# Kernel tuning notes

Measured on AMD Instinct MI355X. Metric: run time of the kernel, lower is better.

Reference implementation:

```python
import jax, jax.numpy as jnp
import numpy as np

FEAT_DIM = 128
GUIDE_DIM = 128
HIDDEN = [1024, 512, 256, 128]
OUT_DIM = 2


def make_coord(shape):
    # grid-center coords in (-1, 1), matching the torch make_coord
    seqs = [(-1.0 + 1.0 / n) + (2.0 / n) * jnp.arange(n, dtype=jnp.float32) for n in shape]
    yy, xx = jnp.meshgrid(seqs[0], seqs[1], indexing='ij')
    return jnp.stack([yy, xx], axis=-1)  # [h, w, 2]


def grid_sample_nearest(img, coord):
    # img: [B, C, H, W]; coord: [B, N, 2] with coord[...,0] along H, coord[...,1] along W
    # replicates F.grid_sample(img, coord.flip(-1)..., mode='nearest', align_corners=False,
    # padding_mode='zeros') followed by permute -> [B, N, C]
    B, C, H, W = img.shape
    iy = jnp.round(((coord[..., 0] + 1.0) * H - 1.0) * 0.5)
    ix = jnp.round(((coord[..., 1] + 1.0) * W - 1.0) * 0.5)
    valid = (iy >= 0) & (iy < H) & (ix >= 0) & (ix < W)
    iyc = jnp.clip(iy, 0, H - 1).astype(jnp.int32)
    ixc = jnp.clip(ix, 0, W - 1).astype(jnp.int32)
    g = jax.vmap(lambda im, y, x: im[:, y, x])(img, iyc, ixc)  # [B, C, N]
    g = g * valid[:, None, :].astype(img.dtype)  # zero padding outside
    return jnp.transpose(g, (0, 2, 1))  # [B, N, C]


def mlp(x, params):
    for W, b in params[:-1]:
        x = jax.nn.relu(x @ W + b)
    W, b = params[-1]
    return x @ W + b


def setup_inputs() -> dict:
    key = jax.random.key(0)
    ks = jax.random.split(key, 16)
    B, h, w = 4, 64, 64
    H_hr = W_hr = 256
    N = H_hr * W_hr  # 65536 query points
    feat = jax.random.normal(ks[0], (B, FEAT_DIM, h, w), jnp.float32)
    coord = jax.random.uniform(ks[1], (B, N, 2), jnp.float32, minval=-1.0, maxval=1.0)
    hr_guide = jax.random.normal(ks[2], (B, GUIDE_DIM, H_hr, W_hr), jnp.float32)
    lr_guide = jax.random.normal(ks[3], (B, GUIDE_DIM, h, w), jnp.float32)
    in_dim = FEAT_DIM + 2 * GUIDE_DIM + 2  # 386
    dims = [in_dim] + HIDDEN + [OUT_DIM]
    inp = {"feat": feat, "coord": coord, "hr_guide": hr_guide, "lr_guide": lr_guide}
    for i in range(len(dims) - 1):
        scale = 1.0 / np.sqrt(dims[i]).astype(np.float32)
        inp[f"W{i}"] = jax.random.normal(ks[4 + 2 * i], (dims[i], dims[i + 1]), jnp.float32) * scale
        inp[f"b{i}"] = jnp.zeros((dims[i + 1],), jnp.float32)
    return inp


def reference(feat, coord, hr_guide, lr_guide, W0, b0, W1, b1, W2, b2, W3, b3, W4, b4):
    params = [(W0, b0), (W1, b1), (W2, b2), (W3, b3), (W4, b4)]
    B, C, h, w = feat.shape
    N = coord.shape[1]
    fc = make_coord((h, w))  # [h, w, 2]
    feat_coord = jnp.broadcast_to(jnp.transpose(fc, (2, 0, 1))[None], (B, 2, h, w))
    q_guide_hr = grid_sample_nearest(hr_guide, coord)  # [B, N, G]
    rx = 1.0 / h
    ry = 1.0 / w
    hw = jnp.array([h, w], dtype=coord.dtype)
    preds = []
    for vx in (-1.0, 1.0):
        for vy in (-1.0, 1.0):
            shift = jnp.array([vx * rx, vy * ry], dtype=coord.dtype)
            coord_ = coord + shift
            q_feat = grid_sample_nearest(feat, coord_)        # [B, N, C]
            q_coord = grid_sample_nearest(feat_coord, coord_)  # [B, N, 2]
            rel_coord = (coord - q_coord) * hw                 # [B, N, 2]
            q_guide_lr = grid_sample_nearest(lr_guide, coord_)  # [B, N, G]
            inp = jnp.concatenate([q_feat, q_guide_hr, q_guide_hr - q_guide_lr, rel_coord], axis=-1)
            pred = mlp(inp.reshape(B * N, -1), params).reshape(B, N, OUT_DIM)
            preds.append(pred)
    preds = jnp.stack(preds, axis=-1)  # [B, N, 2, 4]
    weight = jax.nn.softmax(preds[:, :, 1, :], axis=-1)  # [B, N, 4]
    ret = jnp.sum(preds[:, :, 0, :] * weight, axis=-1, keepdims=True)  # [B, N, 1]
    return ret
```

## Files before the change

### kernel.cpp

```cpp
#include <hip/hip_runtime.h>
#include <cstdint>
#include <cstddef>


typedef unsigned short u16;
typedef unsigned int u32;
typedef _Float16 half8 __attribute__((ext_vector_type(8)));
typedef float floatx4 __attribute__((ext_vector_type(4)));
typedef float floatx2 __attribute__((ext_vector_type(2)));
typedef u32 u32x2 __attribute__((ext_vector_type(2)));
typedef u32 u32x4 __attribute__((ext_vector_type(4)));

__device__ __forceinline__ u16 f2h(float x) {
    _Float16 h = (_Float16)x;
    return __builtin_bit_cast(unsigned short, h);
}
__device__ __forceinline__ float h2f(u16 u) {
    return (float)__builtin_bit_cast(_Float16, u);
}

__device__ __forceinline__ void cp_async16(const void* gsrc, void* lds) {
#if defined(__has_builtin) && __has_builtin(__builtin_amdgcn_global_load_lds)
    __builtin_amdgcn_global_load_lds(
        (__attribute__((address_space(1))) void*)(uintptr_t)gsrc,
        (__attribute__((address_space(3))) void*)(uint32_t)(uintptr_t)lds,
        16, 0, 0);
#else
    *(u32x4*)lds = *(const u32x4*)gsrc;
#endif
}

__global__ void transpose_chw_hwc(const float* __restrict__ src,
                                  u16* __restrict__ dst, int HW) {
    __shared__ float t[32][33];
    const int b = blockIdx.z;
    const int hw0 = blockIdx.x * 32, c0 = blockIdx.y * 32;
    const float* s = src + (size_t)b * 128 * HW;
    u16* d = dst + (size_t)b * HW * 128;
    const int tx = threadIdx.x, ty = threadIdx.y;
#pragma unroll
    for (int j = 0; j < 4; ++j)
        t[ty + j * 8][tx] = s[(size_t)(c0 + ty + j * 8) * HW + hw0 + tx];
    __syncthreads();
#pragma unroll
    for (int j = 0; j < 4; ++j)
        d[(size_t)(hw0 + ty + j * 8) * 128 + c0 + tx] = f2h(t[tx][ty + j * 8]);
}

__global__ void prep_wt(const float* __restrict__ W, u16* __restrict__ Wt,
                        int K, int N, int perm) {
    int idx = blockIdx.x * 256 + threadIdx.x;
    if (idx >= N * K) return;
    int nn = idx / K, kk = idx - nn * K;
    int ka = kk;
    if (perm) {
        int s = kk & 63;
        ka = (kk & ~63) + ((s & 3) << 4) + (s >> 2);
    }
    Wt[idx] = f2h(W[(size_t)ka * N + nn]);
}

__global__ __launch_bounds__(256) void gather_build(
    const float* __restrict__ coord, const u16* __restrict__ hrT,
    const u16* __restrict__ featT, const u16* __restrict__ lrT,
    u16* __restrict__ X, float* __restrict__ rel, int p0) {
    const int wid = threadIdx.x >> 6, lane = threadIdx.x & 63;
    const int pl = blockIdx.x * 4 + wid;
    const int p = p0 + pl;
    const int b = p >> 16;
    const float cy = coord[(size_t)p * 2];
    const float cx = coord[(size_t)p * 2 + 1];
    const u32* hr32 = (const u32*)hrT;
    const u32* ft32 = (const u32*)featT;
    const u32* lr32 = (const u32*)lrT;

    float fy = rintf(((cy + 1.0f) * 256.0f - 1.0f) * 0.5f);
    float fx = rintf(((cx + 1.0f) * 256.0f - 1.0f) * 0.5f);
    bool vh = (fy >= 0.0f) && (fy < 256.0f) && (fx >= 0.0f) && (fx < 256.0f);
    int iy = (int)fminf(fmaxf(fy, 0.0f), 255.0f);
    int ix = (int)fminf(fmaxf(fx, 0.0f), 255.0f);
    u32 hrv = hr32[((((size_t)b * 256 + iy) * 256 + ix) * 128 >> 1) + lane];
    if (!vh) hrv = 0u;
    const float hr_lo = h2f((u16)(hrv & 0xffffu));
    const float hr_hi = h2f((u16)(hrv >> 16));

    const size_t rowbase = (size_t)pl * 4;
#pragma unroll
    for (int s = 0; s < 4; ++s) {
        float sy = (s & 2) ? 0.015625f : -0.015625f;
        float sx = (s & 1) ? 0.015625f : -0.015625f;
        float gy = rintf(((cy + sy + 1.0f) * 64.0f - 1.0f) * 0.5f);
        float gx = rintf(((cx + sx + 1.0f) * 64.0f - 1.0f) * 0.5f);
        bool v = (gy >= 0.0f) && (gy < 64.0f) && (gx >= 0.0f) && (gx < 64.0f);
        int jy = (int)fminf(fmaxf(gy, 0.0f), 63.0f);
        int jx = (int)fminf(fmaxf(gx, 0.0f), 63.0f);
        size_t g32 = ((((size_t)b * 64 + jy) * 64 + jx) * 128 >> 1) + lane;
        u32 fv = ft32[g32];
        u32 lv = lr32[g32];
        if (!v) { fv = 0u; lv = 0u; }
        u16 d_lo = f2h(hr_lo - h2f((u16)(lv & 0xffffu)));
        u16 d_hi = f2h(hr_hi - h2f((u16)(lv >> 16)));

        u32* xr = (u32*)(X + (rowbase + s) * 384);
        xr[lane] = fv;
        xr[64 + lane] = hrv;
        xr[128 + lane] = (u32)d_lo | ((u32)d_hi << 16);

        if (lane == 0) {
            float qcy = v ? (-0.984375f + 0.03125f * (float)jy) : 0.0f;
            float qcx = v ? (-0.984375f + 0.03125f * (float)jx) : 0.0f;
            rel[(rowbase + s) * 2 + 0] = (cy - qcy) * 64.0f;
            rel[(rowbase + s) * 2 + 1] = (cx - qcx) * 64.0f;
        }
    }
}

__global__ __launch_bounds__(512, 2) void gemm_f16_256(
    const u16* __restrict__ A, const u16* __restrict__ Bt,
    const float* __restrict__ bias, u16* __restrict__ C, int K, int N,
    int lognb, const float* __restrict__ rel, const float* __restrict__ w0tail) {
    __shared__ __align__(16) u16 sA[2][2][8192];
    __shared__ __align__(16) u16 sB[2][2][8192];
    const int tid = threadIdx.x;
    const int lane = tid & 63;
    const int wid = tid >> 6;
    const int r = lane & 15, q = lane >> 4;
    const int wm = wid >> 2, wn = wid & 3;

    const int g = blockIdx.x;
    const int n_idx = (g >> 3) & ((1 << lognb) - 1);
    const int m_idx = (g & 7) + ((g >> (3 + lognb)) << 3);
    const int n0 = n_idx << 8;
    const u32 m0 = (u32)m_idx << 8;

    const u32 srow = (u32)(tid >> 2);
    const u32 gchunk = (u32)((tid & 3) ^ ((tid >> 3) & 3));
    const u32 gaoff = (m0 + srow) * (u32)K + (gchunk << 3);
    const u32 gboff = ((u32)n0 + srow) * (u32)K + (gchunk << 3);

    auto stageA = [&](int kt, int ks, int buf) {
        const u16* gp = A + gaoff + (u32)((kt << 6) + (ks << 5));
        u16* lp = &sA[buf][ks][tid << 3];
        cp_async16(gp, lp);
        cp_async16(gp + ((u32)K << 7), lp + 4096);
    };
    auto stageB = [&](int kt, int ks, int buf) {
        const u16* gp = Bt + gboff + (u32)((kt << 6) + (ks << 5));
        u16* lp = &sB[buf][ks][tid << 3];
        cp_async16(gp, lp);
        cp_async16(gp + ((u32)K << 7), lp + 4096);
    };

    const int fs = (q ^ ((r >> 1) & 3)) << 3;
    const int abase = ((wm << 7) + r) * 32 + fs;
    const int bbase = ((wn << 6) + r) * 32 + fs;

    floatx4 acc[8][4];
#pragma unroll
    for (int mi = 0; mi < 8; ++mi)
#pragma unroll
        for (int ni = 0; ni < 4; ++ni)
            acc[mi][ni] = (floatx4){0.0f, 0.0f, 0.0f, 0.0f};

    const int nk = K >> 6;
    stageA(0, 0, 0);
    stageA(0, 1, 0);
    stageB(0, 0, 0);
    stageB(0, 1, 0);
    const int k1 = (nk > 1) ? 1 : 0;
    stageA(k1, 0, 1);
    stageA(k1, 1, 1);
    stageB(k1, 1, 1);
    asm volatile("s_waitcnt vmcnt(6)");
    __builtin_amdgcn_s_barrier();

    for (int kt = 0; kt < nk; ++kt) {
        const int cur = kt & 1, nxt = cur ^ 1;
        const bool p1 = (kt + 1) < nk;
        const bool p2 = (kt + 2) < nk;
        half8 a0[8], a1[8], bf[2];
#pragma unroll
        for (int mi = 0; mi < 8; ++mi)
            a0[mi] = *(const half8*)&sA[cur][0][abase + (mi << 9)];
#pragma unroll
        for (int ni = 0; ni < 2; ++ni)
            bf[ni] = *(const half8*)&sB[cur][0][bbase + (ni << 9)];
        if (p1) stageB(kt + 1, 0, nxt);
        __builtin_amdgcn_s_barrier();
        asm volatile("s_waitcnt lgkmcnt(0)");
        __builtin_amdgcn_s_setprio(1);
#pragma unroll
        for (int mi = 0; mi < 8; ++mi)
#pragma unroll
            for (int ni = 0; ni < 2; ++ni)
                acc[mi][ni] = __builtin_amdgcn_mfma_f32_16x16x32_f16(
                    a0[mi], bf[ni], acc[mi][ni], 0, 0, 0);
        __builtin_amdgcn_s_setprio(0);
        __builtin_amdgcn_s_barrier();
#pragma unroll
        for (int mi = 0; mi < 8; ++mi)
            a1[mi] = *(const half8*)&sA[cur][1][abase + (mi << 9)];
#pragma unroll
        for (int ni = 0; ni < 2; ++ni)
            bf[ni] = *(const half8*)&sB[cur][1][bbase + (ni << 9)];
        if (p2) stageA(kt + 2, 0, cur);
        __builtin_amdgcn_s_barrier();
        asm volatile("s_waitcnt lgkmcnt(0)");
        __builtin_amdgcn_s_setprio(1);
#pragma unroll
        for (int mi = 0; mi < 8; ++mi)
#pragma unroll
            for (int ni = 0; ni < 2; ++ni)
                acc[mi][ni] = __builtin_amdgcn_mfma_f32_16x16x32_f16(
                    a1[mi], bf[ni], acc[mi][ni], 0, 0, 0);
        __builtin_amdgcn_s_setprio(0);
        __builtin_amdgcn_s_barrier();
#pragma unroll
        for (int ni = 0; ni < 2; ++ni)
            bf[ni] = *(const half8*)&sB[cur][1][bbase + 1024 + (ni << 9)];
        if (p2) stageA(kt + 2, 1, cur);
        __builtin_amdgcn_s_barrier();
        asm volatile("s_waitcnt lgkmcnt(0)");
        __builtin_amdgcn_s_setprio(1);
#pragma unroll
        for (int mi = 0; mi < 8; ++mi)
#pragma unroll
            for (int ni = 0; ni < 2; ++ni)
                acc[mi][2 + ni] = __builtin_amdgcn_mfma_f32_16x16x32_f16(
                    a1[mi], bf[ni], acc[mi][2 + ni], 0, 0, 0);
        __builtin_amdgcn_s_setprio(0);
        __builtin_amdgcn_s_barrier();
#pragma unroll
        for (int ni = 0; ni < 2; ++ni)
            bf[ni] = *(const half8*)&sB[cur][0][bbase + 1024 + (ni << 9)];
        if (p2) stageB(kt + 2, 1, cur);
        __builtin_amdgcn_s_barrier();
        asm volatile("s_waitcnt lgkmcnt(0)");
        __builtin_amdgcn_s_setprio(1);
#pragma unroll
        for (int mi = 0; mi < 8; ++mi)
#pragma unroll
            for (int ni = 0; ni < 2; ++ni)
                acc[mi][2 + ni] = __builtin_amdgcn_mfma_f32_16x16x32_f16(
                    a0[mi], bf[ni], acc[mi][2 + ni], 0, 0, 0);
        __builtin_amdgcn_s_setprio(0);
        if (p2) {
            asm volatile("s_waitcnt vmcnt(6)");
        } else {
            asm volatile("s_waitcnt vmcnt(0)");
        }
        __builtin_amdgcn_s_barrier();
    }

    float bias_v[4], w0a[4], w0b[4];
#pragma unroll
    for (int nig = 0; nig < 4; ++nig) {
        int col = n0 + (wn << 6) + nig * 16 + r;
        bias_v[nig] = bias[col];
        w0a[nig] = rel ? w0tail[col] : 0.0f;
        w0b[nig] = rel ? w0tail[N + col] : 0.0f;
    }
#pragma unroll
    for (int mi = 0; mi < 8; ++mi) {
#pragma unroll
        for (int rr = 0; rr < 4; ++rr) {
            u32 row = m0 + (u32)(wm << 7) + (u32)(mi << 4) + (u32)(q << 2) +
                      (u32)rr;
            float rl0 = 0.0f, rl1 = 0.0f;
            if (rel) {
                floatx2 rl = *(const floatx2*)&rel[(size_t)row * 2];
                rl0 = rl[0];
                rl1 = rl[1];
            }
            u32 pk[2];
#pragma unroll
            for (int h = 0; h < 2; ++h) {
                u32 w = 0;
#pragma unroll
                for (int j = 0; j < 2; ++j) {
                    int nig = h * 2 + j;
                    float v = acc[mi][nig][rr] + bias_v[nig];
                    if (rel) v += rl0 * w0a[nig] + rl1 * w0b[nig];
                    v = fmaxf(v, 0.0f);
                    w |= (u32)f2h(v) << (16 * j);
                }
                pk[h] = w;
            }
            *(u32x2*)(C + row * (u32)N + (u32)(n0 + (wn << 6) + (r << 2))) =
                (u32x2){pk[0], pk[1]};
        }
    }
}

__global__ __launch_bounds__(256, 3) void gemm_f16(
    const u16* __restrict__ A, const u16* __restrict__ Bt,
    const float* __restrict__ bias, u16* __restrict__ C, int K, int N,
    int lognb, const float* __restrict__ rel, const float* __restrict__ w0tail) {
    __shared__ __align__(16) u16 As[2][128 * 64];
    __shared__ __align__(16) u16 Bs[128 * 64];
    const int tid = threadIdx.x;
    const int lane = tid & 63;
    const int wid = tid >> 6;
    const int r = lane & 15, q = lane >> 4;
    const int wm = (wid & 1) << 6, wn = (wid >> 1) << 6;

    const int g = blockIdx.x;
    const int n_idx = (g >> 3) & ((1 << lognb) - 1);
    const int m_idx = (g & 7) + ((g >> (3 + lognb)) << 3);
    const int n0 = n_idx << 7;
    const u32 m0 = (u32)m_idx << 7;

    const int srow = tid >> 3;
    const int schunk = (tid & 7) ^ (srow & 7);
    const u32 gaoff = (m0 + (u32)srow) * (u32)K + ((u32)schunk << 3);
    const u32 gboff = (u32)(n0 + srow) * (u32)K + ((u32)schunk << 3);

    auto stageA = [&](int kt, int buf) {
        const u16* gak = A + gaoff + (kt << 6);
        u16* la = &As[buf][tid * 8];
#pragma unroll
        for (int i = 0; i < 4; ++i)
            cp_async16(gak + (u32)(i << 5) * (u32)K, la + (i << 11));
    };

    u32x4 breg[4];
    auto loadB = [&](int kt) {
        const u16* gbk = Bt + gboff + (kt << 6);
#pragma unroll
        for (int i = 0; i < 4; ++i)
            breg[i] = *(const u32x4*)(gbk + (u32)(i << 5) * (u32)K);
    };
    auto writeB = [&]() {
        u16* lb = &Bs[tid * 8];
#pragma unroll
        for (int i = 0; i < 4; ++i)
            *(u32x4*)(lb + (i << 11)) = breg[i];
    };

    const int cx = (q ^ (r & 7)) << 3;
    const int arow = (wm + r) << 6, brow = (wn + r) << 6;

    floatx4 acc[4][4];
#pragma unroll
    for (int mi = 0; mi < 4; ++mi)
#pragma unroll
        for (int ni = 0; ni < 4; ++ni)
            acc[mi][ni] = (floatx4){0.0f, 0.0f, 0.0f, 0.0f};

    const int nk = K >> 6;
    loadB(0);
    stageA(0, 0);
    writeB();
    __syncthreads();

    for (int kt = 0; kt < nk; ++kt) {
        const int cur = kt & 1;
        const bool pf = (kt + 1 < nk);
        if (pf) {
            loadB(kt + 1);
            stageA(kt + 1, cur ^ 1);
        }
#pragma unroll
        for (int ks = 0; ks < 2; ++ks) {
            half8 af[4], bfr[4];
#pragma unroll
            for (int mi = 0; mi < 4; ++mi)
                af[mi] = *(const half8*)&As[cur][arow + (mi << 10) + (cx ^ (ks << 5))];
#pragma unroll
            for (int ni = 0; ni < 4; ++ni)
                bfr[ni] = *(const half8*)&Bs[brow + (ni << 10) + (cx ^ (ks << 5))];
#pragma unroll
            for (int mi = 0; mi < 4; ++mi)
#pragma unroll
                for (int ni = 0; ni < 4; ++ni)
                    acc[mi][ni] = __builtin_amdgcn_mfma_f32_16x16x32_f16(
                        af[mi], bfr[ni], acc[mi][ni], 0, 0, 0);
        }
        if (pf) {
            __syncthreads();
            writeB();
            __syncthreads();
        }
    }

    float bias_v[4], w0a[4], w0b[4];
#pragma unroll
    for (int ni = 0; ni < 4; ++ni) {
        int col = n0 + wn + ni * 16 + r;
        bias_v[ni] = bias[col];
        w0a[ni] = rel ? w0tail[col] : 0.0f;
        w0b[ni] = rel ? w0tail[N + col] : 0.0f;
    }
#pragma unroll
    for (int mi = 0; mi < 4; ++mi) {
#pragma unroll
        for (int rr = 0; rr < 4; ++rr) {
            u32 row = m0 + wm + mi * 16 + q * 4 + rr;
            float rl0 = 0.0f, rl1 = 0.0f;
            if (rel) {
                floatx2 rl = *(const floatx2*)&rel[(size_t)row * 2];
                rl0 = rl[0];
                rl1 = rl[1];
            }
            u32 pk[2];
#pragma unroll
            for (int h = 0; h < 2; ++h) {
                u32 w = 0;
#pragma unroll
                for (int j = 0; j < 2; ++j) {
                    int ni = h * 2 + j;
                    float v = acc[mi][ni][rr] + bias_v[ni];
                    if (rel) v += rl0 * w0a[ni] + rl1 * w0b[ni];
                    v = fmaxf(v, 0.0f);
                    w |= (u32)f2h(v) << (16 * j);
                }
                pk[h] = w;
            }
            *(u32x2*)(C + row * (u32)N + (u32)(n0 + wn + (r << 2))) =
                (u32x2){pk[0], pk[1]};
        }
    }
}

__global__ __launch_bounds__(256) void l4_combine(
    const u16* __restrict__ A3, const float* __restrict__ W4,
    const float* __restrict__ b4, float* __restrict__ out, int p0) {
    const int wid = threadIdx.x >> 6, lane = threadIdx.x & 63;
    const int pl = blockIdx.x * 4 + wid;
    const int p2 = lane * 2;
    const int s0 = p2 & 63, bb = p2 & ~63;
    const int k0 = bb + ((s0 & 3) << 4) + (s0 >> 2);
    const int s1 = s0 + 1;
    const int k1 = bb + ((s1 & 3) << 4) + (s1 >> 2);
    const float w00 = W4[k0 * 2], w01 = W4[k0 * 2 + 1];
    const float w10 = W4[k1 * 2], w11 = W4[k1 * 2 + 1];
    float P0[4], P1[4];
#pragma unroll
    for (int s = 0; s < 4; ++s) {
        size_t rowoff = ((size_t)pl * 4 + s) * 128 + p2;
        u32 av = *(const u32*)(A3 + rowoff);
        float a0 = h2f((u16)(av & 0xffffu));
        float a1 = h2f((u16)(av >> 16));
        float d0 = a0 * w00 + a1 * w10;
        float d1 = a0 * w01 + a1 * w11;
#pragma unroll
        for (int m = 32; m >= 1; m >>= 1) {
            d0 += __shfl_xor(d0, m, 64);
            d1 += __shfl_xor(d1, m, 64);
        }
        P0[s] = d0 + b4[0];
        P1[s] = d1 + b4[1];
    }
    if (lane == 0) {
        float mx = fmaxf(fmaxf(P1[0], P1[1]), fmaxf(P1[2], P1[3]));
        float e0 = __expf(P1[0] - mx), e1 = __expf(P1[1] - mx);
        float e2 = __expf(P1[2] - mx), e3 = __expf(P1[3] - mx);
        float se = e0 + e1 + e2 + e3;
        out[p0 + pl] = (P0[0] * e0 + P0[1] * e1 + P0[2] * e2 + P0[3] * e3) / se;
    }
}

extern "C" void kernel_launch(void* const* d_in, const int* in_sizes, int n_in,
                              void* d_out, int out_size, void* d_ws,
                              size_t ws_size, hipStream_t stream) {
    const float* feat = (const float*)d_in[0];
    const float* coord = (const float*)d_in[1];
    const float* hr = (const float*)d_in[2];
    const float* lr = (const float*)d_in[3];
    const float* W0 = (const float*)d_in[4];
    const float* b0 = (const float*)d_in[5];
    const float* W1 = (const float*)d_in[6];
    const float* b1 = (const float*)d_in[7];
    const float* W2 = (const float*)d_in[8];
    const float* b2 = (const float*)d_in[9];
    const float* W3 = (const float*)d_in[10];
    const float* b3 = (const float*)d_in[11];
    const float* W4 = (const float*)d_in[12];
    const float* b4 = (const float*)d_in[13];
    float* out = (float*)d_out;

    char* base = (char*)d_ws;
    size_t off = 0;
    auto carve = [&](size_t bytes) -> char* {
        char* p = base + off;
        off += (bytes + 255) & ~(size_t)255;
        return p;
    };

    u16* hrT = (u16*)carve(4ull * 65536 * 128 * 2);
    u16* featT = (u16*)carve(4ull * 4096 * 128 * 2);
    u16* lrT = (u16*)carve(4ull * 4096 * 128 * 2);
    u16* Wt0 = (u16*)carve(1024ull * 384 * 2);
    u16* Wt1 = (u16*)carve(512ull * 1024 * 2);
    u16* Wt2 = (u16*)carve(256ull * 512 * 2);
    u16* Wt3 = (u16*)carve(128ull * 256 * 2);
    const size_t fixed = off;

    const size_t R = 1048576ull;
    int c = 16;
    for (; c < 8192; c *= 2) {
        size_t Rc = R / c;
        size_t need = fixed;
        size_t sizes[3] = {Rc * 1024, Rc * 8, Rc * 2048};
        for (int i = 0; i < 3; ++i) need += (sizes[i] + 255) & ~(size_t)255;
        if (need <= ws_size) break;
    }
    const size_t Rc = R / c;
    const int Pc = (int)(262144 / c);

    char* R1 = carve(Rc * 1024);
    float* rel = (float*)carve(Rc * 8);
    char* R2 = carve(Rc * 2048);
    u16* X = (u16*)R1;
    u16* A1 = (u16*)R1;
    u16* A0 = (u16*)R2;
    u16* A2 = (u16*)R2;
    u16* A3 = (u16*)(R2 + Rc * 512);

    transpose_chw_hwc<<<dim3(2048, 4, 4), dim3(32, 8), 0, stream>>>(hr, hrT, 65536);
    transpose_chw_hwc<<<dim3(128, 4, 4), dim3(32, 8), 0, stream>>>(feat, featT, 4096);
    transpose_chw_hwc<<<dim3(128, 4, 4), dim3(32, 8), 0, stream>>>(lr, lrT, 4096);
    prep_wt<<<(1024 * 384 + 255) / 256, 256, 0, stream>>>(W0, Wt0, 384, 1024, 0);
    prep_wt<<<(512 * 1024 + 255) / 256, 256, 0, stream>>>(W1, Wt1, 1024, 512, 1);
    prep_wt<<<(256 * 512 + 255) / 256, 256, 0, stream>>>(W2, Wt2, 512, 256, 1);
    prep_wt<<<(128 * 256 + 255) / 256, 256, 0, stream>>>(W3, Wt3, 256, 128, 1);

    const int mt1 = (int)(Rc / 128);
    const int mt2 = (int)(Rc / 256);
    const bool use256 = (Rc % 2048ull) == 0;
    for (int ci = 0; ci < c; ++ci) {
        const int p0 = ci * Pc;
        gather_build<<<Pc / 4, 256, 0, stream>>>(coord, hrT, featT, lrT, X, rel, p0);
        gemm_f16<<<mt1 * 8, 256, 0, stream>>>(X, Wt0, b0, A0, 384, 1024, 3, rel,
                                              W0 + 384 * 1024);
        if (use256) {
            gemm_f16_256<<<mt2 * 2, 512, 0, stream>>>(A0, Wt1, b1, A1, 1024, 512,
                                                      1, nullptr, nullptr);
            gemm_f16_256<<<mt2 * 1, 512, 0, stream>>>(A1, Wt2, b2, A2, 512, 256,
                                                      0, nullptr, nullptr);
        } else {
            gemm_f16<<<mt1 * 4, 256, 0, stream>>>(A0, Wt1, b1, A1, 1024, 512, 2,
                                                  nullptr, nullptr);
            gemm_f16<<<mt1 * 2, 256, 0, stream>>>(A1, Wt2, b2, A2, 512, 256, 1,
                                                  nullptr, nullptr);
        }
        gemm_f16<<<mt1 * 1, 256, 0, stream>>>(A2, Wt3, b3, A3, 256, 128, 0,
                                              nullptr, nullptr);
        l4_combine<<<Pc / 4, 256, 0, stream>>>(A3, W4, b4, out, p0);
    }
}
```

Measured before the change: 3.718 ms.

## Factor shared hr-guide term out of layer 0 and fuse layers 3-4 with combine

Layer 0 is split algebraically: the hr-guide contribution (W0 hr rows plus diff rows) depends only on the query point, not on the four shifts, so it is computed once per point with a K=128 GEMM. Its result is added in the epilogue of a K=256 GEMM over [feat, lr] using negated diff weights. This cuts layer-0 MACs and the width of the gathered rows. Separately, the layer-3 GEMM is fused with the final 128->2 projection and the softmax combine, which removes the A3 round trip and the l4_combine launch. The cost is an extra launch, an fp16 intermediate H that adds rounding, and extra epilogue loads.

```diff
diff --git a/kernel.cpp b/kernel.cpp
--- a/kernel.cpp
+++ b/kernel.cpp
@@ -60,10 +60,27 @@
     Wt[idx] = f2h(W[(size_t)ka * N + nn]);
 }
 
+__global__ void prep_w0(const float* __restrict__ W0, u16* __restrict__ Wt0m,
+                        u16* __restrict__ Wthr) {
+    int idx = blockIdx.x * 256 + threadIdx.x;
+    if (idx < 1024 * 256) {
+        int n = idx >> 8, k = idx & 255;
+        float v = (k < 128) ? W0[(size_t)k * 1024 + n]
+                            : -W0[(size_t)(128 + k) * 1024 + n];
+        Wt0m[idx] = f2h(v);
+    }
+    if (idx < 1024 * 128) {
+        int n = idx >> 7, k = idx & 127;
+        Wthr[idx] = f2h(W0[(size_t)(128 + k) * 1024 + n] +
+                        W0[(size_t)(256 + k) * 1024 + n]);
+    }
+}
+
 __global__ __launch_bounds__(256) void gather_build(
     const float* __restrict__ coord, const u16* __restrict__ hrT,
     const u16* __restrict__ featT, const u16* __restrict__ lrT,
-    u16* __restrict__ X, float* __restrict__ rel, int p0) {
+    u16* __restrict__ X, u16* __restrict__ Qhr, float* __restrict__ rel,
+    int p0) {
     const int wid = threadIdx.x >> 6, lane = threadIdx.x & 63;
     const int pl = blockIdx.x * 4 + wid;
     const int p = p0 + pl;
@@ -81,8 +98,7 @@
     int ix = (int)fminf(fmaxf(fx, 0.0f), 255.0f);
     u32 hrv = hr32[((((size_t)b * 256 + iy) * 256 + ix) * 128 >> 1) + lane];
     if (!vh) hrv = 0u;
-    const float hr_lo = h2f((u16)(hrv & 0xffffu));
-    const float hr_hi = h2f((u16)(hrv >> 16));
+    ((u32*)Qhr)[(size_t)pl * 64 + lane] = hrv;
 
     const size_t rowbase = (size_t)pl * 4;
 #pragma unroll
@@ -98,13 +114,10 @@
         u32 fv = ft32[g32];
         u32 lv = lr32[g32];
         if (!v) { fv = 0u; lv = 0u; }
-        u16 d_lo = f2h(hr_lo - h2f((u16)(lv & 0xffffu)));
-        u16 d_hi = f2h(hr_hi - h2f((u16)(lv >> 16)));
-
-        u32* xr = (u32*)(X + (rowbase + s) * 384);
+
+        u32* xr = (u32*)(X + (rowbase + s) * 256);
         xr[lane] = fv;
-        xr[64 + lane] = hrv;
-        xr[128 + lane] = (u32)d_lo | ((u32)d_hi << 16);
+        xr[64 + lane] = lv;
 
         if (lane == 0) {
             float qcy = v ? (-0.984375f + 0.03125f * (float)jy) : 0.0f;
@@ -295,7 +308,8 @@
 __global__ __launch_bounds__(256, 3) void gemm_f16(
     const u16* __restrict__ A, const u16* __restrict__ Bt,
     const float* __restrict__ bias, u16* __restrict__ C, int K, int N,
-    int lognb, const float* __restrict__ rel, const float* __restrict__ w0tail) {
+    int lognb, const float* __restrict__ rel, const float* __restrict__ w0tail,
+    const u16* __restrict__ hq, int doRelu) {
     __shared__ __align__(16) u16 As[2][128 * 64];
     __shared__ __align__(16) u16 Bs[128 * 64];
     const int tid = threadIdx.x;
@@ -387,12 +401,25 @@
 #pragma unroll
     for (int ni = 0; ni < 4; ++ni) {
         int col = n0 + wn + ni * 16 + r;
-        bias_v[ni] = bias[col];
+        bias_v[ni] = bias ? bias[col] : 0.0f;
         w0a[ni] = rel ? w0tail[col] : 0.0f;
         w0b[ni] = rel ? w0tail[N + col] : 0.0f;
     }
 #pragma unroll
     for (int mi = 0; mi < 4; ++mi) {
+        float addv[4];
+        if (hq) {
+            u32 pidx = ((m0 + (u32)wm + (u32)(mi << 4)) >> 2) + (u32)q;
+            u32x2 hv = *(const u32x2*)(hq + (size_t)pidx * (u32)N +
+                                       (u32)(n0 + wn + (r << 2)));
+            addv[0] = h2f((u16)(hv[0] & 0xffffu));
+            addv[1] = h2f((u16)(hv[0] >> 16));
+            addv[2] = h2f((u16)(hv[1] & 0xffffu));
+            addv[3] = h2f((u16)(hv[1] >> 16));
+        } else {
+#pragma unroll
+            for (int ni = 0; ni < 4; ++ni) addv[ni] = bias_v[ni];
+        }
 #pragma unroll
         for (int rr = 0; rr < 4; ++rr) {
             u32 row = m0 + wm + mi * 16 + q * 4 + rr;
@@ -409,9 +436,9 @@
 #pragma unroll
                 for (int j = 0; j < 2; ++j) {
                     int ni = h * 2 + j;
-                    float v = acc[mi][ni][rr] + bias_v[ni];
+                    float v = acc[mi][ni][rr] + addv[ni];
                     if (rel) v += rl0 * w0a[ni] + rl1 * w0b[ni];
-                    v = fmaxf(v, 0.0f);
+                    if (doRelu) v = fmaxf(v, 0.0f);
                     w |= (u32)f2h(v) << (16 * j);
                 }
                 pk[h] = w;
@@ -422,41 +449,142 @@
     }
 }
 
-__global__ __launch_bounds__(256) void l4_combine(
-    const u16* __restrict__ A3, const float* __restrict__ W4,
+__global__ __launch_bounds__(256, 3) void gemm_l3l4(
+    const u16* __restrict__ A, const u16* __restrict__ Bt,
+    const float* __restrict__ b3, const float* __restrict__ W4,
     const float* __restrict__ b4, float* __restrict__ out, int p0) {
-    const int wid = threadIdx.x >> 6, lane = threadIdx.x & 63;
-    const int pl = blockIdx.x * 4 + wid;
-    const int p2 = lane * 2;
-    const int s0 = p2 & 63, bb = p2 & ~63;
-    const int k0 = bb + ((s0 & 3) << 4) + (s0 >> 2);
-    const int s1 = s0 + 1;
-    const int k1 = bb + ((s1 & 3) << 4) + (s1 >> 2);
-    const float w00 = W4[k0 * 2], w01 = W4[k0 * 2 + 1];
-    const float w10 = W4[k1 * 2], w11 = W4[k1 * 2 + 1];
-    float P0[4], P1[4];
-#pragma unroll
-    for (int s = 0; s < 4; ++s) {
-        size_t rowoff = ((size_t)pl * 4 + s) * 128 + p2;
-        u32 av = *(const u32*)(A3 + rowoff);
-        float a0 = h2f((u16)(av & 0xffffu));
-        float a1 = h2f((u16)(av >> 16));
-        float d0 = a0 * w00 + a1 * w10;
-        float d1 = a0 * w01 + a1 * w11;
-#pragma unroll
-        for (int m = 32; m >= 1; m >>= 1) {
-            d0 += __shfl_xor(d0, m, 64);
-            d1 += __shfl_xor(d1, m, 64);
-        }
-        P0[s] = d0 + b4[0];
-        P1[s] = d1 + b4[1];
-    }
-    if (lane == 0) {
+    __shared__ __align__(16) u16 As[2][128 * 64];
+    __shared__ __align__(16) u16 Bs[128 * 64];
+    __shared__ float sums[2][2][64][2];
+    const int K = 256;
+    const int tid = threadIdx.x;
+    const int lane = tid & 63;
+    const int wid = tid >> 6;
+    const int r = lane & 15, q = lane >> 4;
+    const int wm1 = wid & 1, wn1 = wid >> 1;
+    const int wm = wm1 << 6, wn = wn1 << 6;
+    const u32 m0 = (u32)blockIdx.x << 7;
+
+    const int srow = tid >> 3;
+    const int schunk = (tid & 7) ^ (srow & 7);
+    const u32 gaoff = (m0 + (u32)srow) * (u32)K + ((u32)schunk << 3);
+    const u32 gboff = (u32)srow * (u32)K + ((u32)schunk << 3);
+
+    auto stageA = [&](int kt, int buf) {
+        const u16* gak = A + gaoff + (kt << 6);
+        u16* la = &As[buf][tid * 8];
+#pragma unroll
+        for (int i = 0; i < 4; ++i)
+            cp_async16(gak + (u32)(i << 5) * (u32)K, la + (i << 11));
+    };
+
+    u32x4 breg[4];
+    auto loadB = [&](int kt) {
+        const u16* gbk = Bt + gboff + (kt << 6);
+#pragma unroll
+        for (int i = 0; i < 4; ++i)
+            breg[i] = *(const u32x4*)(gbk + (u32)(i << 5) * (u32)K);
+    };
+    auto writeB = [&]() {
+        u16* lb = &Bs[tid * 8];
+#pragma unroll
+        for (int i = 0; i < 4; ++i)
+            *(u32x4*)(lb + (i << 11)) = breg[i];
+    };
+
+    const int cx = (q ^ (r & 7)) << 3;
+    const int arow = (wm + r) << 6, brow = (wn + r) << 6;
+
+    floatx4 acc[4][4];
+#pragma unroll
+    for (int mi = 0; mi < 4; ++mi)
+#pragma unroll
+        for (int ni = 0; ni < 4; ++ni)
+            acc[mi][ni] = (floatx4){0.0f, 0.0f, 0.0f, 0.0f};
+
+    const int nk = K >> 6;
+    loadB(0);
+    stageA(0, 0);
+    writeB();
+    __syncthreads();
+    for (int kt = 0; kt < nk; ++kt) {
+        const int cur = kt & 1;
+        const bool pf = (kt + 1 < nk);
+        if (pf) {
+            loadB(kt + 1);
+            stageA(kt + 1, cur ^ 1);
+        }
+#pragma unroll
+        for (int ks = 0; ks < 2; ++ks) {
+            half8 af[4], bfr[4];
+#pragma unroll
+            for (int mi = 0; mi < 4; ++mi)
+                af[mi] = *(const half8*)&As[cur][arow + (mi << 10) + (cx ^ (ks << 5))];
+#pragma unroll
+            for (int ni = 0; ni < 4; ++ni)
+                bfr[ni] = *(const half8*)&Bs[brow + (ni << 10) + (cx ^ (ks << 5))];
+#pragma unroll
+            for (int mi = 0; mi < 4; ++mi)
+#pragma unroll
+                for (int ni = 0; ni < 4; ++ni)
+                    acc[mi][ni] = __builtin_amdgcn_mfma_f32_16x16x32_f16(
+                        af[mi], bfr[ni], acc[mi][ni], 0, 0, 0);
+        }
+        if (pf) {
+            __syncthreads();
+            writeB();
+            __syncthreads();
+        }
+    }
+
+    float b3v[4], w40[4], w41[4];
+#pragma unroll
+    for (int ni = 0; ni < 4; ++ni) {
+        int ch = wn + ni * 16 + r;
+        b3v[ni] = b3[ch];
+        w40[ni] = W4[ch * 2];
+        w41[ni] = W4[ch * 2 + 1];
+    }
+#pragma unroll
+    for (int mi = 0; mi < 4; ++mi) {
+#pragma unroll
+        for (int rr = 0; rr < 4; ++rr) {
+            float d0 = 0.0f, d1 = 0.0f;
+#pragma unroll
+            for (int ni = 0; ni < 4; ++ni) {
+                float v = fmaxf(acc[mi][ni][rr] + b3v[ni], 0.0f);
+                d0 += v * w40[ni];
+                d1 += v * w41[ni];
+            }
+#pragma unroll
+            for (int m = 1; m <= 8; m <<= 1) {
+                d0 += __shfl_xor(d0, m, 64);
+                d1 += __shfl_xor(d1, m, 64);
+            }
+            if (r == 0) {
+                int rl = mi * 16 + q * 4 + rr;
+                sums[wm1][wn1][rl][0] = d0;
+                sums[wm1][wn1][rl][1] = d1;
+            }
+        }
+    }
+    __syncthreads();
+    if (tid < 32) {
+        const int pl = tid;
+        const int w = pl >> 4;
+        const int rb = (pl & 15) * 4;
+        float P0[4], P1[4];
+#pragma unroll
+        for (int s = 0; s < 4; ++s) {
+            P0[s] = sums[w][0][rb + s][0] + sums[w][1][rb + s][0] + b4[0];
+            P1[s] = sums[w][0][rb + s][1] + sums[w][1][rb + s][1] + b4[1];
+        }
         float mx = fmaxf(fmaxf(P1[0], P1[1]), fmaxf(P1[2], P1[3]));
         float e0 = __expf(P1[0] - mx), e1 = __expf(P1[1] - mx);
         float e2 = __expf(P1[2] - mx), e3 = __expf(P1[3] - mx);
         float se = e0 + e1 + e2 + e3;
-        out[p0 + pl] = (P0[0] * e0 + P0[1] * e1 + P0[2] * e2 + P0[3] * e3) / se;
+        out[p0 + (int)(m0 >> 2) + pl] =
+            (P0[0] * e0 + P0[1] * e1 + P0[2] * e2 + P0[3] * e3) / se;
     }
 }
 
@@ -490,7 +618,8 @@
     u16* hrT = (u16*)carve(4ull * 65536 * 128 * 2);
     u16* featT = (u16*)carve(4ull * 4096 * 128 * 2);
     u16* lrT = (u16*)carve(4ull * 4096 * 128 * 2);
-    u16* Wt0 = (u16*)carve(1024ull * 384 * 2);
+    u16* Wt0m = (u16*)carve(1024ull * 256 * 2);
+    u16* Wthr = (u16*)carve(1024ull * 128 * 2);
     u16* Wt1 = (u16*)carve(512ull * 1024 * 2);
     u16* Wt2 = (u16*)carve(256ull * 512 * 2);
     u16* Wt3 = (u16*)carve(128ull * 256 * 2);
@@ -512,27 +641,32 @@
     float* rel = (float*)carve(Rc * 8);
     char* R2 = carve(Rc * 2048);
     u16* X = (u16*)R1;
+    u16* H = (u16*)(R1 + Rc * 512);
     u16* A1 = (u16*)R1;
+    u16* Qhr = (u16*)R2;
     u16* A0 = (u16*)R2;
     u16* A2 = (u16*)R2;
-    u16* A3 = (u16*)(R2 + Rc * 512);
 
     transpose_chw_hwc<<<dim3(2048, 4, 4), dim3(32, 8), 0, stream>>>(hr, hrT, 65536);
     transpose_chw_hwc<<<dim3(128, 4, 4), dim3(32, 8), 0, stream>>>(feat, featT, 4096);
     transpose_chw_hwc<<<dim3(128, 4, 4), dim3(32, 8), 0, stream>>>(lr, lrT, 4096);
-    prep_wt<<<(1024 * 384 + 255) / 256, 256, 0, stream>>>(W0, Wt0, 384, 1024, 0);
+    prep_w0<<<1024, 256, 0, stream>>>(W0, Wt0m, Wthr);
     prep_wt<<<(512 * 1024 + 255) / 256, 256, 0, stream>>>(W1, Wt1, 1024, 512, 1);
     prep_wt<<<(256 * 512 + 255) / 256, 256, 0, stream>>>(W2, Wt2, 512, 256, 1);
     prep_wt<<<(128 * 256 + 255) / 256, 256, 0, stream>>>(W3, Wt3, 256, 128, 1);
 
     const int mt1 = (int)(Rc / 128);
     const int mt2 = (int)(Rc / 256);
+    const int mth = (int)(Rc / 512);
     const bool use256 = (Rc % 2048ull) == 0;
     for (int ci = 0; ci < c; ++ci) {
         const int p0 = ci * Pc;
-        gather_build<<<Pc / 4, 256, 0, stream>>>(coord, hrT, featT, lrT, X, rel, p0);
-        gemm_f16<<<mt1 * 8, 256, 0, stream>>>(X, Wt0, b0, A0, 384, 1024, 3, rel,
-                                              W0 + 384 * 1024);
+        gather_build<<<Pc / 4, 256, 0, stream>>>(coord, hrT, featT, lrT, X, Qhr,
+                                                 rel, p0);
+        gemm_f16<<<mth * 8, 256, 0, stream>>>(Qhr, Wthr, b0, H, 128, 1024, 3,
+                                              nullptr, nullptr, nullptr, 0);
+        gemm_f16<<<mt1 * 8, 256, 0, stream>>>(X, Wt0m, nullptr, A0, 256, 1024,
+                                              3, rel, W0 + 384 * 1024, H, 1);
         if (use256) {
             gemm_f16_256<<<mt2 * 2, 512, 0, stream>>>(A0, Wt1, b1, A1, 1024, 512,
                                                       1, nullptr, nullptr);
@@ -540,12 +674,10 @@
                                                       0, nullptr, nullptr);
         } else {
             gemm_f16<<<mt1 * 4, 256, 0, stream>>>(A0, Wt1, b1, A1, 1024, 512, 2,
-                                                  nullptr, nullptr);
+                                                  nullptr, nullptr, nullptr, 1);
             gemm_f16<<<mt1 * 2, 256, 0, stream>>>(A1, Wt2, b2, A2, 512, 256, 1,
-                                                  nullptr, nullptr);
-        }
-        gemm_f16<<<mt1 * 1, 256, 0, stream>>>(A2, Wt3, b3, A3, 256, 128, 0,
-                                              nullptr, nullptr);
-        l4_combine<<<Pc / 4, 256, 0, stream>>>(A3, W4, b4, out, p0);
-    }
-}
+                                                  nullptr, nullptr, nullptr, 1);
+        }
+        gemm_l3l4<<<mt1, 256, 0, stream>>>(A2, Wt3, b3, W4, b4, out, p0);
+    }
+}
```

New measurement: 3.404 ms. -8.5%, faster.
